# Kernel tuning notes

Hardware: AMD Instinct MI355X
Metric: run time of the kernel (lower is better)

The kernel has to match this reference:

```python
import jax, jax.numpy as jnp
import numpy as np

NUM_HEADS = 12

def setup_inputs() -> dict:
    key = jax.random.key(0)
    k1, k2, k3 = jax.random.split(key, 3)
    B, N, C = 8, 1024, 768
    x = jax.random.normal(k1, (B, N, C), dtype=jnp.float32)
    Wqkv = jax.random.normal(k2, (C, 3 * C), dtype=jnp.float32) * (C ** -0.5)
    bqkv = jnp.zeros((3 * C,), dtype=jnp.float32)
    Wproj = jax.random.normal(k3, (C, C), dtype=jnp.float32) * (C ** -0.5)
    bproj = jnp.zeros((C,), dtype=jnp.float32)
    return {"x": x, "Wqkv": Wqkv, "bqkv": bqkv, "Wproj": Wproj, "bproj": bproj}

def reference(x, Wqkv, bqkv, Wproj, bproj):
    B, N, C = x.shape
    H = NUM_HEADS
    D = C // H
    scale = D ** -0.5
    qkv = x @ Wqkv + bqkv                       # [B,N,3C]
    qkv = qkv.reshape(B, N, 3, H, D)
    q, k, v = qkv[:, :, 0], qkv[:, :, 1], qkv[:, :, 2]  # [B,N,H,D]
    attn = jnp.einsum('bnhd,bmhd->bhnm', q, k) * scale  # [B,H,N,N]
    attn = jax.nn.softmax(attn, axis=-1)
    # dropout is identity in eval mode
    out = jnp.einsum('bhnm,bmhd->bnhd', attn, v).reshape(B, N, C)
    out = out @ Wproj + bproj
    return out
```

## Files before the change

### kernel.cpp

```cpp
#include <hip/hip_runtime.h>
#include <hip/hip_bf16.h>
#include <cstdint>
#include <cstddef>

typedef __bf16 bf16;
typedef __bf16 bf16x8 __attribute__((ext_vector_type(8)));
typedef __bf16 bf16x4 __attribute__((ext_vector_type(4)));
typedef __bf16 bf16x2 __attribute__((ext_vector_type(2)));
typedef float f32x4 __attribute__((ext_vector_type(4)));
typedef float f32x16 __attribute__((ext_vector_type(16)));
typedef unsigned int u32;
typedef u32 u32x4 __attribute__((ext_vector_type(4)));

#define LDS_CAST(p) (__attribute__((address_space(3))) void*)(p)
#define GLB_CAST(p) (const __attribute__((address_space(1))) void*)(p)
#define MFMA16(a, b, c) __builtin_amdgcn_mfma_f32_16x16x32_bf16(a, b, c, 0, 0, 0)
#define MFMA32(a, b, c) __builtin_amdgcn_mfma_f32_32x32x16_bf16(a, b, c, 0, 0, 0)

#if __has_builtin(__builtin_amdgcn_exp2f)
#define EXPF(x) __builtin_amdgcn_exp2f(x)
#define QK_SCALE 0.18033688011112042f
#else
#define EXPF(x) __expf(x)
#define QK_SCALE 0.125f
#endif

static constexpr int BATCH = 8;
static constexpr int NSEQ  = 1024;
static constexpr int CDIM  = 768;
static constexpr int NH    = 12;
static constexpr int HD    = 64;
static constexpr int MTOT  = BATCH * NSEQ;
static constexpr int NC3   = 3 * CDIM;

__device__ inline u32 pkbf(float a, float b) {
    bf16x2 t = { (bf16)a, (bf16)b };
    return __builtin_bit_cast(u32, t);
}

__global__ void cast_kernel(const float* __restrict__ src, bf16* __restrict__ dst, int n4) {
    int i = blockIdx.x * blockDim.x + threadIdx.x;
    if (i < n4) {
        float4 v = ((const float4*)src)[i];
        bf16x4 o = { (bf16)v.x, (bf16)v.y, (bf16)v.z, (bf16)v.w };
        ((bf16x4*)dst)[i] = o;
    }
}

__global__ void tcast_kernel(const float* __restrict__ src, bf16* __restrict__ dst,
                             int K, int N) {
    int k = blockIdx.x * blockDim.x + threadIdx.x;
    int n = blockIdx.y;
    if (k < K) dst[(size_t)n * K + k] = (bf16)src[(size_t)k * N + n];
}

template <int MODE>
__global__ __launch_bounds__(256) void gemm_kernel(
    const bf16* __restrict__ A, const bf16* __restrict__ Bt,
    const float* __restrict__ bias, float* __restrict__ outf,
    bf16* __restrict__ q, bf16* __restrict__ kk, bf16* __restrict__ v,
    int Ndim, int K)
{
    __shared__ alignas(16) bf16 sA[128 * 32];
    __shared__ alignas(16) bf16 sB[128 * 32];
    const int tid  = threadIdx.x;
    const int lane = tid & 63;
    const int wid  = tid >> 6;
    const int quad = lane >> 4;
    const int l16  = lane & 15;
    const int wm   = (wid >> 1) * 64;
    const int wn   = (wid & 1) * 64;
    const int tm   = blockIdx.y * 128;
    const int tn   = blockIdx.x * 128;

    const f32x4 fzero = {0.f, 0.f, 0.f, 0.f};
    f32x4 acc[4][4];
#pragma unroll
    for (int i = 0; i < 4; i++)
#pragma unroll
        for (int j = 0; j < 4; j++) acc[i][j] = fzero;

    const int srow = tid >> 2;
    const int sk8  = (tid & 3) * 8;
    const bf16* gA = A  + (size_t)(tm + srow) * K + sk8;
    const bf16* gB = Bt + (size_t)(tn + srow) * K + sk8;
    const size_t rs64 = (size_t)64 * K;
    bf16* dA0 = sA + wid * 512;
    bf16* dA1 = sA + 2048 + wid * 512;
    bf16* dB0 = sB + wid * 512;
    bf16* dB1 = sB + 2048 + wid * 512;

    for (int k0 = 0; k0 < K; k0 += 32) {
        __syncthreads();
        __builtin_amdgcn_global_load_lds(GLB_CAST(gA + k0),        LDS_CAST(dA0), 16, 0, 0);
        __builtin_amdgcn_global_load_lds(GLB_CAST(gA + rs64 + k0), LDS_CAST(dA1), 16, 0, 0);
        __builtin_amdgcn_global_load_lds(GLB_CAST(gB + k0),        LDS_CAST(dB0), 16, 0, 0);
        __builtin_amdgcn_global_load_lds(GLB_CAST(gB + rs64 + k0), LDS_CAST(dB1), 16, 0, 0);
        __syncthreads();

        bf16x8 af[4], bfr[4];
#pragma unroll
        for (int i = 0; i < 4; i++)
            af[i] = *(const bf16x8*)(sA + (wm + i * 16 + l16) * 32 + quad * 8);
#pragma unroll
        for (int i = 0; i < 4; i++)
            bfr[i] = *(const bf16x8*)(sB + (wn + i * 16 + l16) * 32 + quad * 8);
#pragma unroll
        for (int i = 0; i < 4; i++)
#pragma unroll
            for (int j = 0; j < 4; j++) acc[i][j] = MFMA16(af[i], bfr[j], acc[i][j]);
    }

    if (MODE == 0) {
#pragma unroll
        for (int i = 0; i < 4; i++) {
            int row = tm + wm + i * 16 + quad * 4;
#pragma unroll
            for (int j = 0; j < 4; j++) {
                int col = tn + wn + j * 16 + l16;
                float bv = bias[col];
                float* op = outf + (size_t)row * Ndim + col;
#pragma unroll
                for (int r = 0; r < 4; r++) op[(size_t)r * Ndim] = acc[i][j][r] + bv;
            }
        }
    } else {
#pragma unroll
        for (int i = 0; i < 4; i++) {
            int row = tm + wm + i * 16 + quad * 4;
            int b  = row >> 10;
            int ns = row & 1023;
#pragma unroll
            for (int j = 0; j < 4; j++) {
                int col = tn + wn + j * 16 + l16;
                int t3  = col / 768;
                int rem = col - t3 * 768;
                int h = rem >> 6;
                int d = rem & 63;
                float bv = bias[col];
                if (t3 == 0) {
                    bf16* qp = q + ((size_t)(b * NH + h) * NSEQ + ns) * HD + d;
#pragma unroll
                    for (int r = 0; r < 4; r++)
                        qp[(size_t)r * HD] = (bf16)((acc[i][j][r] + bv) * (float)QK_SCALE);
                } else if (t3 == 1) {
                    bf16* kp = kk + ((size_t)(b * NH + h) * NSEQ + ns) * HD + d;
#pragma unroll
                    for (int r = 0; r < 4; r++) kp[(size_t)r * HD] = (bf16)(acc[i][j][r] + bv);
                } else {
                    bf16x4 pv = { (bf16)(acc[i][j][0] + bv), (bf16)(acc[i][j][1] + bv),
                                  (bf16)(acc[i][j][2] + bv), (bf16)(acc[i][j][3] + bv) };
                    *(bf16x4*)(v + ((size_t)(b * NH + h) * HD + d) * NSEQ + ns) = pv;
                }
            }
        }
    }
}

__global__ __launch_bounds__(256) void attn_kernel(
    const bf16* __restrict__ q, const bf16* __restrict__ k,
    const bf16* __restrict__ v, bf16* __restrict__ o)
{
    __shared__ alignas(16) bf16 sQ[128 * 64];
    __shared__ alignas(16) bf16 sK[2][64 * 64];
    __shared__ alignas(16) bf16 sV[2][64 * 64];
    const int tid  = threadIdx.x;
    const int lane = tid & 63;
    const int w    = tid >> 6;
    const int h    = lane >> 5;
    const int l32  = lane & 31;
    const int qt = blockIdx.x;
    const int bh = blockIdx.y;
    const int b = bh / NH, hh = bh - b * NH;

    const bf16* qb = q + ((size_t)bh * NSEQ + qt * 128) * HD;
    const bf16* kb = k + (size_t)bh * NSEQ * HD;
    const bf16* vb = v + (size_t)bh * HD * NSEQ;

#pragma unroll
    for (int i = 0; i < 4; i++) {
        int slot = w * 256 + i * 64 + lane;
        int r = slot >> 3, cs = slot & 7;
        __builtin_amdgcn_global_load_lds(GLB_CAST(qb + r * HD + ((cs ^ (r & 7)) * 8)),
                                         LDS_CAST(sQ + (w * 256 + i * 64) * 8), 16, 0, 0);
    }
    auto stageKV = [&](int kt, int buf) {
#pragma unroll
        for (int i = 0; i < 2; i++) {
            int slot = w * 128 + i * 64 + lane;
            int r = slot >> 3, cs = slot & 7;
            int cc = (cs ^ (r & 7)) * 8;
            __builtin_amdgcn_global_load_lds(GLB_CAST(kb + (size_t)(kt * 64 + r) * HD + cc),
                                             LDS_CAST(&sK[buf][(w * 128 + i * 64) * 8]), 16, 0, 0);
            __builtin_amdgcn_global_load_lds(GLB_CAST(vb + (size_t)r * NSEQ + kt * 64 + cc),
                                             LDS_CAST(&sV[buf][(w * 128 + i * 64) * 8]), 16, 0, 0);
        }
    };
    stageKV(0, 0);
    __syncthreads();

    bf16x8 qf[4];
    {
        int row = w * 32 + l32, rx = row & 7;
#pragma unroll
        for (int cd = 0; cd < 4; cd++)
            qf[cd] = *(const bf16x8*)(sQ + (row * 8 + ((2 * cd + h) ^ rx)) * 8);
    }

    f32x16 accO[2];
#pragma unroll
    for (int dt = 0; dt < 2; dt++)
#pragma unroll
        for (int i = 0; i < 16; i++) accO[dt][i] = 0.f;
    float m_run = -3e38f, l_run = 0.f;

    for (int kt = 0; kt < 16; kt++) {
        const int cur = kt & 1;
        __syncthreads();
        if (kt < 15) stageKV(kt + 1, 1 - cur);
        const bf16* sKc = sK[cur];
        const bf16* sVc = sV[cur];

        f32x16 accS[2];
#pragma unroll
        for (int kvt = 0; kvt < 2; kvt++)
#pragma unroll
            for (int i = 0; i < 16; i++) accS[kvt][i] = 0.f;
#pragma unroll
        for (int kvt = 0; kvt < 2; kvt++) {
            int row = kvt * 32 + l32, rx = row & 7;
#pragma unroll
            for (int cd = 0; cd < 4; cd++) {
                bf16x8 kf = *(const bf16x8*)(sKc + (row * 8 + ((2 * cd + h) ^ rx)) * 8);
                accS[kvt] = MFMA32(kf, qf[cd], accS[kvt]);
            }
        }

        float tmv[16];
#pragma unroll
        for (int i = 0; i < 16; i++) tmv[i] = fmaxf(accS[0][i], accS[1][i]);
#pragma unroll
        for (int s = 8; s >= 1; s >>= 1)
#pragma unroll
            for (int i = 0; i < s; i++) tmv[i] = fmaxf(tmv[i], tmv[i + s]);
        float tmax = fmaxf(tmv[0], __shfl_xor(tmv[0], 32));
        float mnew = fmaxf(m_run, tmax);
        float alpha = EXPF(m_run - mnew);
        m_run = mnew;

        float tsv[16];
#pragma unroll
        for (int kvt = 0; kvt < 2; kvt++)
#pragma unroll
            for (int i = 0; i < 16; i++) {
                float p = EXPF(accS[kvt][i] - mnew);
                accS[kvt][i] = p;
            }
#pragma unroll
        for (int i = 0; i < 16; i++) tsv[i] = accS[0][i] + accS[1][i];
#pragma unroll
        for (int s = 8; s >= 1; s >>= 1)
#pragma unroll
            for (int i = 0; i < s; i++) tsv[i] += tsv[i + s];
        float rs = tsv[0] + __shfl_xor(tsv[0], 32);
        l_run = l_run * alpha + rs;
#pragma unroll
        for (int dt = 0; dt < 2; dt++)
#pragma unroll
            for (int i = 0; i < 16; i++) accO[dt][i] *= alpha;

        u32 pr[2][4][2];
#pragma unroll
        for (int kvt = 0; kvt < 2; kvt++)
#pragma unroll
            for (int g = 0; g < 4; g++) {
                pr[kvt][g][0] = pkbf(accS[kvt][4 * g + 0], accS[kvt][4 * g + 1]);
                pr[kvt][g][1] = pkbf(accS[kvt][4 * g + 2], accS[kvt][4 * g + 3]);
            }
        bf16x8 pf[4];
#pragma unroll
        for (int c = 0; c < 4; c++) {
            int kvt = c >> 1, c1 = c & 1;
            u32 u00 = pr[kvt][2 * c1][0],     u01 = pr[kvt][2 * c1][1];
            u32 u10 = pr[kvt][2 * c1 + 1][0], u11 = pr[kvt][2 * c1 + 1][1];
            u32 y0 = h ? u10 : u00, y1 = h ? u11 : u01;
            u32 z0 = h ? u00 : u10, z1 = h ? u01 : u11;
            u32 w0 = (u32)__shfl_xor((int)z0, 32);
            u32 w1 = (u32)__shfl_xor((int)z1, 32);
            u32x4 fv = { h ? w0 : y0, h ? w1 : y1, h ? y0 : w0, h ? y1 : w1 };
            pf[c] = __builtin_bit_cast(bf16x8, fv);
        }

#pragma unroll
        for (int dt = 0; dt < 2; dt++) {
            int row = dt * 32 + l32, rx = row & 7;
#pragma unroll
            for (int c = 0; c < 4; c++) {
                bf16x8 vf = *(const bf16x8*)(sVc + (row * 8 + ((2 * c + h) ^ rx)) * 8);
                accO[dt] = MFMA32(vf, pf[c], accO[dt]);
            }
        }
    }

    float inv = 1.f / l_run;
    bf16* ob = o + ((size_t)b * NSEQ + qt * 128 + w * 32 + l32) * CDIM + hh * HD;
#pragma unroll
    for (int dt = 0; dt < 2; dt++)
#pragma unroll
        for (int g = 0; g < 4; g++) {
            bf16x4 t = { (bf16)(accO[dt][4 * g + 0] * inv), (bf16)(accO[dt][4 * g + 1] * inv),
                         (bf16)(accO[dt][4 * g + 2] * inv), (bf16)(accO[dt][4 * g + 3] * inv) };
            *(bf16x4*)(ob + dt * 32 + 8 * g + 4 * h) = t;
        }
}

extern "C" void kernel_launch(void* const* d_in, const int* in_sizes, int n_in,
                              void* d_out, int out_size, void* d_ws, size_t ws_size,
                              hipStream_t stream)
{
    const float* x     = (const float*)d_in[0];
    const float* Wqkv  = (const float*)d_in[1];
    const float* bqkv  = (const float*)d_in[2];
    const float* Wproj = (const float*)d_in[3];
    const float* bproj = (const float*)d_in[4];
    float* out = (float*)d_out;

    char* ws = (char*)d_ws;
    const size_t MC2 = (size_t)MTOT * CDIM * 2;
    bf16* xb     = (bf16*)ws; ws += MC2;
    bf16* wqkvt  = (bf16*)ws; ws += (size_t)NC3 * CDIM * 2;
    bf16* wprojt = (bf16*)ws; ws += (size_t)CDIM * CDIM * 2;
    bf16* qw     = (bf16*)ws; ws += MC2;
    bf16* kw     = (bf16*)ws; ws += MC2;
    bf16* vw     = (bf16*)ws; ws += MC2;
    bf16* ow     = (bf16*)ws; ws += MC2;

    int n4 = MTOT * CDIM / 4;
    cast_kernel<<<dim3((n4 + 255) / 256), dim3(256), 0, stream>>>(x, xb, n4);
    tcast_kernel<<<dim3(3, NC3),  dim3(256), 0, stream>>>(Wqkv,  wqkvt,  CDIM, NC3);
    tcast_kernel<<<dim3(3, CDIM), dim3(256), 0, stream>>>(Wproj, wprojt, CDIM, CDIM);

    gemm_kernel<1><<<dim3(NC3 / 128, MTOT / 128), dim3(256), 0, stream>>>(
        xb, wqkvt, bqkv, nullptr, qw, kw, vw, NC3, CDIM);

    attn_kernel<<<dim3(NSEQ / 128, BATCH * NH), dim3(256), 0, stream>>>(qw, kw, vw, ow);

    gemm_kernel<0><<<dim3(CDIM / 128, MTOT / 128), dim3(256), 0, stream>>>(
        ow, wprojt, bproj, out, nullptr, nullptr, nullptr, CDIM, CDIM);
}
```

Baseline: 225.3 us.

## Pipeline GEMM with triple-buffered LDS, swizzle, larger tiles, tiled weight transpose

```diff
diff --git a/kernel.cpp b/kernel.cpp
--- a/kernel.cpp
+++ b/kernel.cpp
@@ -49,29 +49,63 @@
 
 __global__ void tcast_kernel(const float* __restrict__ src, bf16* __restrict__ dst,
                              int K, int N) {
-    int k = blockIdx.x * blockDim.x + threadIdx.x;
-    int n = blockIdx.y;
-    if (k < K) dst[(size_t)n * K + k] = (bf16)src[(size_t)k * N + n];
+    __shared__ float tile[32][33];
+    const int n0 = blockIdx.x * 32, k0 = blockIdx.y * 32;
+    const int tx = threadIdx.x & 31, ty = threadIdx.x >> 5;
+#pragma unroll
+    for (int p = 0; p < 4; p++)
+        tile[ty + p * 8][tx] = src[(size_t)(k0 + ty + p * 8) * N + n0 + tx];
+    __syncthreads();
+#pragma unroll
+    for (int p = 0; p < 4; p++)
+        dst[(size_t)(n0 + ty + p * 8) * K + k0 + tx] = (bf16)tile[tx][ty + p * 8];
 }
 
 template <int MODE>
-__global__ __launch_bounds__(256) void gemm_kernel(
+__global__ __launch_bounds__(512, 4) void gemm_kernel(
     const bf16* __restrict__ A, const bf16* __restrict__ Bt,
     const float* __restrict__ bias, float* __restrict__ outf,
     bf16* __restrict__ q, bf16* __restrict__ kk, bf16* __restrict__ v,
     int Ndim, int K)
 {
-    __shared__ alignas(16) bf16 sA[128 * 32];
-    __shared__ alignas(16) bf16 sB[128 * 32];
+    __shared__ alignas(16) bf16 sAB[3][12288];
     const int tid  = threadIdx.x;
     const int lane = tid & 63;
-    const int wid  = tid >> 6;
     const int quad = lane >> 4;
     const int l16  = lane & 15;
-    const int wm   = (wid >> 1) * 64;
-    const int wn   = (wid & 1) * 64;
-    const int tm   = blockIdx.y * 128;
-    const int tn   = blockIdx.x * 128;
+    const int wid  = tid >> 6;
+    const int wmI  = wid >> 1;
+    const int wnI  = wid & 1;
+
+    const int wg = blockIdx.x;
+    const int x  = (wg & 7) * (gridDim.x >> 3) + (wg >> 3);
+    const int nTn = Ndim >> 7;
+    const int tn = x % nTn, tm = x / nTn;
+    const int tmB = tm << 8, tnB = tn << 7;
+
+    int aoff[4], boff[4];
+    {
+        const int xr = ((quad ^ (l16 & 3)) << 3);
+#pragma unroll
+        for (int i = 0; i < 4; i++) aoff[i] = (wmI * 64 + i * 16 + l16) * 32 + xr;
+#pragma unroll
+        for (int j = 0; j < 4; j++) boff[j] = 8192 + (wnI * 64 + j * 16 + l16) * 32 + xr;
+    }
+
+    const int r0 = tid >> 2;
+    const int c0 = (tid & 3) ^ (r0 & 3);
+    const bf16* gA0 = A  + (size_t)(tmB + r0) * K + c0 * 8;
+    const bf16* gA1 = gA0 + (size_t)128 * K;
+    const bf16* gB0 = Bt + (size_t)(tnB + r0) * K + c0 * 8;
+    const int ldsb = (tid & 448) * 8;
+
+    auto STAGE = [&](int t, int bsel) {
+        const int k0 = t << 5;
+        bf16* d = &sAB[bsel][0];
+        __builtin_amdgcn_global_load_lds(GLB_CAST(gA0 + k0), LDS_CAST(d + ldsb),        16, 0, 0);
+        __builtin_amdgcn_global_load_lds(GLB_CAST(gA1 + k0), LDS_CAST(d + 4096 + ldsb), 16, 0, 0);
+        __builtin_amdgcn_global_load_lds(GLB_CAST(gB0 + k0), LDS_CAST(d + 8192 + ldsb), 16, 0, 0);
+    };
 
     const f32x4 fzero = {0.f, 0.f, 0.f, 0.f};
     f32x4 acc[4][4];
@@ -80,44 +114,49 @@
 #pragma unroll
         for (int j = 0; j < 4; j++) acc[i][j] = fzero;
 
-    const int srow = tid >> 2;
-    const int sk8  = (tid & 3) * 8;
-    const bf16* gA = A  + (size_t)(tm + srow) * K + sk8;
-    const bf16* gB = Bt + (size_t)(tn + srow) * K + sk8;
-    const size_t rs64 = (size_t)64 * K;
-    bf16* dA0 = sA + wid * 512;
-    bf16* dA1 = sA + 2048 + wid * 512;
-    bf16* dB0 = sB + wid * 512;
-    bf16* dB1 = sB + 2048 + wid * 512;
-
-    for (int k0 = 0; k0 < K; k0 += 32) {
-        __syncthreads();
-        __builtin_amdgcn_global_load_lds(GLB_CAST(gA + k0),        LDS_CAST(dA0), 16, 0, 0);
-        __builtin_amdgcn_global_load_lds(GLB_CAST(gA + rs64 + k0), LDS_CAST(dA1), 16, 0, 0);
-        __builtin_amdgcn_global_load_lds(GLB_CAST(gB + k0),        LDS_CAST(dB0), 16, 0, 0);
-        __builtin_amdgcn_global_load_lds(GLB_CAST(gB + rs64 + k0), LDS_CAST(dB1), 16, 0, 0);
-        __syncthreads();
-
+    const int NT = K >> 5;
+    STAGE(0, 0);
+    STAGE(1, 1);
+    asm volatile("s_waitcnt vmcnt(3)" ::: "memory");
+    __builtin_amdgcn_sched_barrier(0);
+    __builtin_amdgcn_s_barrier();
+
+    int bsel = 0;
+    for (int t = 0; t < NT; ++t) {
+        int b2 = bsel + 2; if (b2 >= 3) b2 -= 3;
+        if (t + 2 < NT) STAGE(t + 2, b2);
+
+        const bf16* buf = &sAB[bsel][0];
         bf16x8 af[4], bfr[4];
 #pragma unroll
+        for (int i = 0; i < 4; i++) af[i]  = *(const bf16x8*)(buf + aoff[i]);
+#pragma unroll
+        for (int j = 0; j < 4; j++) bfr[j] = *(const bf16x8*)(buf + boff[j]);
+
+        __builtin_amdgcn_s_setprio(1);
+#pragma unroll
         for (int i = 0; i < 4; i++)
-            af[i] = *(const bf16x8*)(sA + (wm + i * 16 + l16) * 32 + quad * 8);
-#pragma unroll
-        for (int i = 0; i < 4; i++)
-            bfr[i] = *(const bf16x8*)(sB + (wn + i * 16 + l16) * 32 + quad * 8);
-#pragma unroll
-        for (int i = 0; i < 4; i++)
 #pragma unroll
             for (int j = 0; j < 4; j++) acc[i][j] = MFMA16(af[i], bfr[j], acc[i][j]);
+        __builtin_amdgcn_s_setprio(0);
+
+        if (t < NT - 1) {
+            if (t + 2 < NT) asm volatile("s_waitcnt vmcnt(3)" ::: "memory");
+            else            asm volatile("s_waitcnt vmcnt(0)" ::: "memory");
+            __builtin_amdgcn_sched_barrier(0);
+            __builtin_amdgcn_s_barrier();
+            __builtin_amdgcn_sched_barrier(0);
+        }
+        bsel += 1; if (bsel >= 3) bsel -= 3;
     }
 
     if (MODE == 0) {
 #pragma unroll
         for (int i = 0; i < 4; i++) {
-            int row = tm + wm + i * 16 + quad * 4;
+            int row = tmB + wmI * 64 + i * 16 + quad * 4;
 #pragma unroll
             for (int j = 0; j < 4; j++) {
-                int col = tn + wn + j * 16 + l16;
+                int col = tnB + wnI * 64 + j * 16 + l16;
                 float bv = bias[col];
                 float* op = outf + (size_t)row * Ndim + col;
 #pragma unroll
@@ -127,12 +166,12 @@
     } else {
 #pragma unroll
         for (int i = 0; i < 4; i++) {
-            int row = tm + wm + i * 16 + quad * 4;
+            int row = tmB + wmI * 64 + i * 16 + quad * 4;
             int b  = row >> 10;
             int ns = row & 1023;
 #pragma unroll
             for (int j = 0; j < 4; j++) {
-                int col = tn + wn + j * 16 + l16;
+                int col = tnB + wnI * 64 + j * 16 + l16;
                 int t3  = col / 768;
                 int rem = col - t3 * 768;
                 int h = rem >> 6;
@@ -337,14 +376,14 @@
 
     int n4 = MTOT * CDIM / 4;
     cast_kernel<<<dim3((n4 + 255) / 256), dim3(256), 0, stream>>>(x, xb, n4);
-    tcast_kernel<<<dim3(3, NC3),  dim3(256), 0, stream>>>(Wqkv,  wqkvt,  CDIM, NC3);
-    tcast_kernel<<<dim3(3, CDIM), dim3(256), 0, stream>>>(Wproj, wprojt, CDIM, CDIM);
-
-    gemm_kernel<1><<<dim3(NC3 / 128, MTOT / 128), dim3(256), 0, stream>>>(
+    tcast_kernel<<<dim3(NC3 / 32, CDIM / 32), dim3(256), 0, stream>>>(Wqkv,  wqkvt,  CDIM, NC3);
+    tcast_kernel<<<dim3(CDIM / 32, CDIM / 32), dim3(256), 0, stream>>>(Wproj, wprojt, CDIM, CDIM);
+
+    gemm_kernel<1><<<dim3((NC3 / 128) * (MTOT / 256)), dim3(512), 0, stream>>>(
         xb, wqkvt, bqkv, nullptr, qw, kw, vw, NC3, CDIM);
 
     attn_kernel<<<dim3(NSEQ / 128, BATCH * NH), dim3(256), 0, stream>>>(qw, kw, vw, ow);
 
-    gemm_kernel<0><<<dim3(CDIM / 128, MTOT / 128), dim3(256), 0, stream>>>(
+    gemm_kernel<0><<<dim3((CDIM / 128) * (MTOT / 256)), dim3(512), 0, stream>>>(
         ow, wprojt, bproj, out, nullptr, nullptr, nullptr, CDIM, CDIM);
 }
```

Measured after the change: 203.0 us. 9.9% less time.
